# Kernel optimization log

Hardware: AMD Instinct MI355X
Metric: run time of the kernel (lower is better)

The kernel has to match this reference:

```python
import jax, jax.numpy as jnp
import numpy as np

E = 16        # num_experts
TOPK = 2      # num_experts_per_tok


def setup_inputs() -> dict:
    key = jax.random.key(0)
    ks = jax.random.split(key, 8)
    B, S, H, I, IS = 4, 2048, 1024, 512, 2048
    std = 0.02
    return {
        "hidden_states": jax.random.normal(ks[0], (B, S, H), jnp.float32),
        "gate_w": jax.random.normal(ks[1], (E, H), jnp.float32) * std,
        "gate_up_proj": jax.random.normal(ks[2], (E, 2 * I, H), jnp.float32) * std,
        "down_proj": jax.random.normal(ks[3], (E, H, I), jnp.float32) * std,
        "shared_gate_proj": jax.random.normal(ks[4], (IS, H), jnp.float32) * std,
        "shared_up_proj": jax.random.normal(ks[5], (IS, H), jnp.float32) * std,
        "shared_down_proj": jax.random.normal(ks[6], (H, IS), jnp.float32) * std,
        "shared_expert_gate_w": jax.random.normal(ks[7], (1, H), jnp.float32) * std,
    }


def _moe(x, gate_w, gate_up_proj, down_proj, sgp, sup, sdp, segw):
    # x: [N, H] flattened tokens
    N = x.shape[0]
    router_logits = x @ gate_w.T                      # [N, E]
    probs = jax.nn.softmax(router_logits, axis=-1)
    routing_weights, selected = jax.lax.top_k(probs, TOPK)   # [N, TOPK]
    routing_weights = routing_weights / routing_weights.sum(-1, keepdims=True)
    # combine weights scattered into dense [N, E] (per-token per-expert gate)
    combine = jnp.zeros((N, E), x.dtype).at[jnp.arange(N)[:, None], selected].add(routing_weights)

    def body(acc, ws):
        gu_w, d_w, cw = ws                            # [2I,H], [H,I], [N]
        gu = x @ gu_w.T                               # [N, 2I]
        g, u = jnp.split(gu, 2, axis=-1)
        h = jax.nn.silu(g) * u                        # [N, I]
        return acc + cw[:, None] * (h @ d_w.T), None

    expert_out, _ = jax.lax.scan(body, jnp.zeros_like(x), (gate_up_proj, down_proj, combine.T))

    # shared expert with sigmoid token gate
    shared_h = jax.nn.silu(x @ sgp.T) * (x @ sup.T)   # [N, IS]
    shared_out = (shared_h @ sdp.T) * jax.nn.sigmoid(x @ segw.T)  # [N, H]
    out = expert_out + shared_out

    # aux (load-balancing) loss
    counts = jnp.sum(jax.nn.one_hot(selected, E, dtype=x.dtype), axis=(0, 1))  # [E]
    frac_tokens = counts / (N * TOPK)
    frac_probs = probs.sum(0) / N
    aux_loss = E * jnp.sum(frac_tokens * frac_probs)
    return out, aux_loss


def reference(hidden_states, gate_w, gate_up_proj, down_proj, shared_gate_proj, shared_up_proj, shared_down_proj, shared_expert_gate_w):
    B, S, H = hidden_states.shape
    out, aux = _moe(hidden_states.reshape(-1, H), gate_w, gate_up_proj, down_proj,
                    shared_gate_proj, shared_up_proj, shared_down_proj, shared_expert_gate_w)
    return out.reshape(B, S, H), aux
```

## Files before the change

kernel.cpp:

```cpp
#include <hip/hip_runtime.h>
#include <hip/hip_bf16.h>
#include <stdint.h>


#define N_TOK 8192
#define HDIM 1024
#define NEXP 16
#define IEXP 512
#define ISH 2048

typedef __bf16 bf16x8 __attribute__((ext_vector_type(8)));
typedef float f32x4 __attribute__((ext_vector_type(4)));

#define OFF_XBF   ((size_t)0)
#define OFF_WSG   ((size_t)16777216)
#define OFF_WSU   ((size_t)20971520)
#define OFF_WSD   ((size_t)25165824)
#define OFF_SH    ((size_t)29360128)
#define OFF_HEXP  ((size_t)62914560)
#define OFF_IDS   ((size_t)79691776)
#define OFF_TW    ((size_t)80216064)
#define OFF_META  ((size_t)80740352)
#define OFF_SIG   ((size_t)80740608)
#define OFF_LG    ((size_t)80773376)

static __device__ __forceinline__ unsigned short f2bf(float f) {
  unsigned int u = __float_as_uint(f);
  u += 0x7fffu + ((u >> 16) & 1u);
  return (unsigned short)(u >> 16);
}
static __device__ __forceinline__ int pack_bf2(float a, float b) {
  return (int)f2bf(a) | ((int)f2bf(b) << 16);
}
static __device__ __forceinline__ void gl_lds16(const void* g, void* l) {
  __builtin_amdgcn_global_load_lds(
      (const __attribute__((address_space(1))) unsigned int*)g,
      (__attribute__((address_space(3))) unsigned int*)l, 16, 0, 0);
}

__global__ void cvt_kernel(const float* __restrict__ src,
                           unsigned short* __restrict__ dst, int n4) {
  int i = blockIdx.x * 256 + threadIdx.x;
  if (i >= n4) return;
  float4 v = ((const float4*)src)[i];
  uint2 o;
  o.x = (unsigned)pack_bf2(v.x, v.y);
  o.y = (unsigned)pack_bf2(v.z, v.w);
  ((uint2*)dst)[i] = o;
}

__global__ __launch_bounds__(256) void logits_kernel(
    const float* __restrict__ X, const float* __restrict__ GW,
    const float* __restrict__ SEGW, float* __restrict__ LG) {
  int wid = threadIdx.x >> 6, lane = threadIdx.x & 63;
  int tok = blockIdx.x * 4 + wid;
  const float* xr = X + (size_t)tok * HDIM;
  float xv[16];
#pragma unroll
  for (int i = 0; i < 16; i++) xv[i] = xr[lane + 64 * i];
  float myv = 0.f;
#pragma unroll
  for (int e = 0; e < 17; e++) {
    const float* wr = (e < 16) ? (GW + (size_t)e * HDIM) : SEGW;
    float p = 0.f;
#pragma unroll
    for (int i = 0; i < 16; i++) p += xv[i] * wr[lane + 64 * i];
#pragma unroll
    for (int off = 32; off >= 1; off >>= 1) p += __shfl_xor(p, off, 64);
    if (lane == e) myv = p;
  }
  if (lane < 17) LG[(size_t)tok * 32 + lane] = myv;
}

__global__ __launch_bounds__(256) void route_kernel(
    const float* __restrict__ LG, int* __restrict__ cnt,
    float* __restrict__ pps, int* __restrict__ ids,
    float* __restrict__ tw, float* __restrict__ sig) {
  __shared__ int lcnt[16];
  __shared__ int lbase[16];
  __shared__ float lps[16];
  int tid = threadIdx.x;
  int tok = blockIdx.x * 256 + tid;
  if (tid < 16) { lcnt[tid] = 0; lps[tid] = 0.f; }
  __syncthreads();
  const float4* row = (const float4*)(LG + (size_t)tok * 32);
  float4 v0 = row[0], v1 = row[1], v2 = row[2], v3 = row[3];
  float g16 = row[4].x;
  float lg[16] = {v0.x, v0.y, v0.z, v0.w, v1.x, v1.y, v1.z, v1.w,
                  v2.x, v2.y, v2.z, v2.w, v3.x, v3.y, v3.z, v3.w};
  float mx = lg[0];
#pragma unroll
  for (int e = 1; e < 16; e++) mx = fmaxf(mx, lg[e]);
  float pr[16], s = 0.f;
#pragma unroll
  for (int e = 0; e < 16; e++) { pr[e] = __expf(lg[e] - mx); s += pr[e]; }
  float inv_s = 1.f / s;
  float p1 = -1.f, p2 = -1.f; int i1 = 0, i2 = 0;
#pragma unroll
  for (int e = 0; e < 16; e++) {
    if (pr[e] > p1) { p2 = p1; i2 = i1; p1 = pr[e]; i1 = e; }
    else if (pr[e] > p2) { p2 = pr[e]; i2 = e; }
  }
  float wsum = p1 + p2;
  int s1 = atomicAdd(&lcnt[i1], 1);
  int s2 = atomicAdd(&lcnt[i2], 1);
#pragma unroll
  for (int e = 0; e < 16; e++) atomicAdd(&lps[e], pr[e] * inv_s);
  sig[tok] = 1.f / (1.f + __expf(-g16));
  __syncthreads();
  if (tid < 16) {
    lbase[tid] = atomicAdd(&cnt[tid], lcnt[tid]);
    atomicAdd(&pps[tid], lps[tid]);
  }
  __syncthreads();
  int d1 = i1 * N_TOK + lbase[i1] + s1;
  int d2 = i2 * N_TOK + lbase[i2] + s2;
  ids[d1] = tok; tw[d1] = p1 / wsum;
  ids[d2] = tok; tw[d2] = p2 / wsum;
}

__global__ void offs_aux_kernel(const int* __restrict__ cnt, int* __restrict__ off,
                                const float* __restrict__ probs_sum,
                                float* __restrict__ out_aux) {
  if (threadIdx.x == 0 && blockIdx.x == 0) {
    int run = 0; float aux = 0.f;
    for (int e = 0; e < NEXP; e++) {
      off[e] = run; run += cnt[e];
      aux += ((float)cnt[e] / (float)(N_TOK * 2)) * (probs_sum[e] / (float)N_TOK);
    }
    off[16] = run;
    *out_aux = (float)NEXP * aux;
  }
}

__global__ __launch_bounds__(256) void shared_gemm1_kernel(
    const unsigned short* __restrict__ X, const unsigned short* __restrict__ Wg,
    const unsigned short* __restrict__ Wu, unsigned short* __restrict__ H) {
  __shared__ __align__(16) unsigned short As[128 * 32];
  __shared__ __align__(16) unsigned short Bs1[64 * 32];
  __shared__ __align__(16) unsigned short Bs2[64 * 32];
  int m0 = blockIdx.y * 128, n0 = blockIdx.x * 64;
  int t = threadIdx.x, lane = t & 63, w = t >> 6;
  int wm = (w & 1) * 64, wn = (w >> 1) * 32;
  int arow = t >> 2, akb = (t & 3) * 8;
  const unsigned short* ap0 = X + (size_t)(m0 + arow) * HDIM + akb;
  const unsigned short* ap1 = X + (size_t)(m0 + 64 + arow) * HDIM + akb;
  const unsigned short* bp1 = Wg + (size_t)(n0 + arow) * HDIM + akb;
  const unsigned short* bp2 = Wu + (size_t)(n0 + arow) * HDIM + akb;
  f32x4 z = {0.f, 0.f, 0.f, 0.f};
  f32x4 accg[4][2], accu[4][2];
#pragma unroll
  for (int i = 0; i < 4; i++)
#pragma unroll
    for (int j = 0; j < 2; j++) { accg[i][j] = z; accu[i][j] = z; }
  for (int k0 = 0; k0 < HDIM; k0 += 32) {
    __syncthreads();
    gl_lds16(ap0 + k0, &As[t * 8]);
    gl_lds16(ap1 + k0, &As[2048 + t * 8]);
    gl_lds16(bp1 + k0, &Bs1[t * 8]);
    gl_lds16(bp2 + k0, &Bs2[t * 8]);
    __syncthreads();
    int fr = lane & 15, fc = (lane >> 4) * 8;
    bf16x8 af[4], bg[2], bu[2];
#pragma unroll
    for (int i = 0; i < 4; i++) af[i] = *(const bf16x8*)&As[(wm + i * 16 + fr) * 32 + fc];
#pragma unroll
    for (int j = 0; j < 2; j++) {
      bg[j] = *(const bf16x8*)&Bs1[(wn + j * 16 + fr) * 32 + fc];
      bu[j] = *(const bf16x8*)&Bs2[(wn + j * 16 + fr) * 32 + fc];
    }
#pragma unroll
    for (int i = 0; i < 4; i++)
#pragma unroll
      for (int j = 0; j < 2; j++) {
        accg[i][j] = __builtin_amdgcn_mfma_f32_16x16x32_bf16(af[i], bg[j], accg[i][j], 0, 0, 0);
        accu[i][j] = __builtin_amdgcn_mfma_f32_16x16x32_bf16(af[i], bu[j], accu[i][j], 0, 0, 0);
      }
  }
  int col = lane & 15, rq = (lane >> 4) * 4;
#pragma unroll
  for (int i = 0; i < 4; i++)
#pragma unroll
    for (int j = 0; j < 2; j++)
#pragma unroll
      for (int r = 0; r < 4; r++) {
        int mm = m0 + wm + i * 16 + rq + r;
        int nn = n0 + wn + j * 16 + col;
        float g = accg[i][j][r], u = accu[i][j][r];
        float h = g / (1.f + __expf(-g)) * u;
        H[(size_t)mm * ISH + nn] = f2bf(h);
      }
}

__global__ __launch_bounds__(256) void shared_gemm2_kernel(
    const unsigned short* __restrict__ H, const unsigned short* __restrict__ Wd,
    const float* __restrict__ sig, float* __restrict__ Out) {
  __shared__ __align__(16) unsigned short As[128 * 32];
  __shared__ __align__(16) unsigned short Bs[128 * 32];
  int m0 = blockIdx.y * 128, n0 = blockIdx.x * 128;
  int t = threadIdx.x, lane = t & 63, w = t >> 6;
  int wm = (w & 1) * 64, wn = (w >> 1) * 64;
  int arow = t >> 2, akb = (t & 3) * 8;
  const unsigned short* apA0 = H + (size_t)(m0 + arow) * ISH + akb;
  const unsigned short* apA1 = H + (size_t)(m0 + 64 + arow) * ISH + akb;
  const unsigned short* apB0 = Wd + (size_t)(n0 + arow) * ISH + akb;
  const unsigned short* apB1 = Wd + (size_t)(n0 + 64 + arow) * ISH + akb;
  f32x4 z = {0.f, 0.f, 0.f, 0.f};
  f32x4 acc[4][4];
#pragma unroll
  for (int i = 0; i < 4; i++)
#pragma unroll
    for (int j = 0; j < 4; j++) acc[i][j] = z;
  for (int k0 = 0; k0 < ISH; k0 += 32) {
    __syncthreads();
    gl_lds16(apA0 + k0, &As[t * 8]);
    gl_lds16(apA1 + k0, &As[2048 + t * 8]);
    gl_lds16(apB0 + k0, &Bs[t * 8]);
    gl_lds16(apB1 + k0, &Bs[2048 + t * 8]);
    __syncthreads();
    int fr = lane & 15, fc = (lane >> 4) * 8;
    bf16x8 af[4], bfr[4];
#pragma unroll
    for (int i = 0; i < 4; i++) {
      af[i] = *(const bf16x8*)&As[(wm + i * 16 + fr) * 32 + fc];
      bfr[i] = *(const bf16x8*)&Bs[(wn + i * 16 + fr) * 32 + fc];
    }
#pragma unroll
    for (int i = 0; i < 4; i++)
#pragma unroll
      for (int j = 0; j < 4; j++)
        acc[i][j] = __builtin_amdgcn_mfma_f32_16x16x32_bf16(af[i], bfr[j], acc[i][j], 0, 0, 0);
  }
  int col = lane & 15, rq = (lane >> 4) * 4;
#pragma unroll
  for (int i = 0; i < 4; i++)
#pragma unroll
    for (int r = 0; r < 4; r++) {
      int mm = m0 + wm + i * 16 + rq + r;
      float sg = sig[mm];
#pragma unroll
      for (int j = 0; j < 4; j++) {
        int nn = n0 + wn + j * 16 + col;
        Out[(size_t)mm * HDIM + nn] = acc[i][j][r] * sg;
      }
    }
}

__global__ __launch_bounds__(256) void exp_gemm1_kernel(
    const unsigned short* __restrict__ X, const float* __restrict__ WGU,
    const int* __restrict__ ids, const int* __restrict__ cnt,
    const int* __restrict__ off, unsigned short* __restrict__ Hexp) {
  int e = blockIdx.z;
  int ne = cnt[e];
  int m0 = blockIdx.y * 128;
  if (m0 >= ne) return;
  __shared__ __align__(16) unsigned short As[128 * 32];
  __shared__ __align__(16) unsigned short Bs1[64 * 32];
  __shared__ __align__(16) unsigned short Bs2[64 * 32];
  int n0 = blockIdx.x * 64;
  const int* eids = ids + e * N_TOK;
  int base = off[e];
  int t = threadIdx.x, lane = t & 63, w = t >> 6;
  int wm = (w & 1) * 64, wn = (w >> 1) * 32;
  int arow = t >> 2, akb = (t & 3) * 8;
  int s0 = m0 + arow, s1 = m0 + 64 + arow;
  int t0 = (s0 < ne) ? eids[s0] : 0;
  int t1 = (s1 < ne) ? eids[s1] : 0;
  const unsigned short* ap0 = X + (size_t)t0 * HDIM + akb;
  const unsigned short* ap1 = X + (size_t)t1 * HDIM + akb;
  const float* bpg = WGU + ((size_t)e * 1024 + n0 + arow) * HDIM + akb;
  const float* bpu = WGU + ((size_t)e * 1024 + 512 + n0 + arow) * HDIM + akb;
  f32x4 z = {0.f, 0.f, 0.f, 0.f};
  f32x4 accg[4][2], accu[4][2];
#pragma unroll
  for (int i = 0; i < 4; i++)
#pragma unroll
    for (int j = 0; j < 2; j++) { accg[i][j] = z; accu[i][j] = z; }
  for (int k0 = 0; k0 < HDIM; k0 += 32) {
    float4 g0 = *(const float4*)(bpg + k0);
    float4 g1 = *(const float4*)(bpg + k0 + 4);
    float4 u0 = *(const float4*)(bpu + k0);
    float4 u1 = *(const float4*)(bpu + k0 + 4);
    int4 b1, b2;
    b1.x = pack_bf2(g0.x, g0.y); b1.y = pack_bf2(g0.z, g0.w);
    b1.z = pack_bf2(g1.x, g1.y); b1.w = pack_bf2(g1.z, g1.w);
    b2.x = pack_bf2(u0.x, u0.y); b2.y = pack_bf2(u0.z, u0.w);
    b2.z = pack_bf2(u1.x, u1.y); b2.w = pack_bf2(u1.z, u1.w);
    __syncthreads();
    gl_lds16(ap0 + k0, &As[t * 8]);
    gl_lds16(ap1 + k0, &As[2048 + t * 8]);
    *(int4*)&Bs1[arow * 32 + akb] = b1;
    *(int4*)&Bs2[arow * 32 + akb] = b2;
    __syncthreads();
    int fr = lane & 15, fc = (lane >> 4) * 8;
    bf16x8 af[4], bg[2], bu[2];
#pragma unroll
    for (int i = 0; i < 4; i++) af[i] = *(const bf16x8*)&As[(wm + i * 16 + fr) * 32 + fc];
#pragma unroll
    for (int j = 0; j < 2; j++) {
      bg[j] = *(const bf16x8*)&Bs1[(wn + j * 16 + fr) * 32 + fc];
      bu[j] = *(const bf16x8*)&Bs2[(wn + j * 16 + fr) * 32 + fc];
    }
#pragma unroll
    for (int i = 0; i < 4; i++)
#pragma unroll
      for (int j = 0; j < 2; j++) {
        accg[i][j] = __builtin_amdgcn_mfma_f32_16x16x32_bf16(af[i], bg[j], accg[i][j], 0, 0, 0);
        accu[i][j] = __builtin_amdgcn_mfma_f32_16x16x32_bf16(af[i], bu[j], accu[i][j], 0, 0, 0);
      }
  }
  int col = lane & 15, rq = (lane >> 4) * 4;
#pragma unroll
  for (int i = 0; i < 4; i++)
#pragma unroll
    for (int j = 0; j < 2; j++)
#pragma unroll
      for (int r = 0; r < 4; r++) {
        int slot = m0 + wm + i * 16 + rq + r;
        if (slot < ne) {
          int nn = n0 + wn + j * 16 + col;
          float g = accg[i][j][r], u = accu[i][j][r];
          float h = g / (1.f + __expf(-g)) * u;
          Hexp[(size_t)(base + slot) * IEXP + nn] = f2bf(h);
        }
      }
}

__global__ __launch_bounds__(256) void exp_gemm2_kernel(
    const unsigned short* __restrict__ Hexp, const float* __restrict__ WD,
    const int* __restrict__ ids, const float* __restrict__ tw,
    const int* __restrict__ cnt, const int* __restrict__ off,
    float* __restrict__ Out) {
  int e = blockIdx.z;
  int ne = cnt[e];
  int m0 = blockIdx.y * 128;
  if (m0 >= ne) return;
  __shared__ __align__(16) unsigned short As[128 * 32];
  __shared__ __align__(16) unsigned short Bs[64 * 32];
  int n0 = blockIdx.x * 64;
  const int* eids = ids + e * N_TOK;
  const float* etw = tw + e * N_TOK;
  int base = off[e];
  int t = threadIdx.x, lane = t & 63, w = t >> 6;
  int wm = (w & 1) * 64, wn = (w >> 1) * 32;
  int arow = t >> 2, akb = (t & 3) * 8;
  int ra0 = base + m0 + arow;        if (ra0 > 16383) ra0 = 16383;
  int ra1 = base + m0 + 64 + arow;   if (ra1 > 16383) ra1 = 16383;
  const unsigned short* ap0 = Hexp + (size_t)ra0 * IEXP + akb;
  const unsigned short* ap1 = Hexp + (size_t)ra1 * IEXP + akb;
  const float* bp = WD + ((size_t)e * HDIM + n0 + arow) * IEXP + akb;
  f32x4 z = {0.f, 0.f, 0.f, 0.f};
  f32x4 acc[4][2];
#pragma unroll
  for (int i = 0; i < 4; i++)
#pragma unroll
    for (int j = 0; j < 2; j++) acc[i][j] = z;
  for (int k0 = 0; k0 < IEXP; k0 += 32) {
    float4 d0 = *(const float4*)(bp + k0);
    float4 d1 = *(const float4*)(bp + k0 + 4);
    int4 b0;
    b0.x = pack_bf2(d0.x, d0.y); b0.y = pack_bf2(d0.z, d0.w);
    b0.z = pack_bf2(d1.x, d1.y); b0.w = pack_bf2(d1.z, d1.w);
    __syncthreads();
    gl_lds16(ap0 + k0, &As[t * 8]);
    gl_lds16(ap1 + k0, &As[2048 + t * 8]);
    *(int4*)&Bs[arow * 32 + akb] = b0;
    __syncthreads();
    int fr = lane & 15, fc = (lane >> 4) * 8;
    bf16x8 af[4], bfr[2];
#pragma unroll
    for (int i = 0; i < 4; i++) af[i] = *(const bf16x8*)&As[(wm + i * 16 + fr) * 32 + fc];
#pragma unroll
    for (int j = 0; j < 2; j++) bfr[j] = *(const bf16x8*)&Bs[(wn + j * 16 + fr) * 32 + fc];
#pragma unroll
    for (int i = 0; i < 4; i++)
#pragma unroll
      for (int j = 0; j < 2; j++)
        acc[i][j] = __builtin_amdgcn_mfma_f32_16x16x32_bf16(af[i], bfr[j], acc[i][j], 0, 0, 0);
  }
  int col = lane & 15, rq = (lane >> 4) * 4;
#pragma unroll
  for (int i = 0; i < 4; i++)
#pragma unroll
    for (int r = 0; r < 4; r++) {
      int slot = m0 + wm + i * 16 + rq + r;
      if (slot < ne) {
        int tok = eids[slot];
        float wgt = etw[slot];
#pragma unroll
        for (int j = 0; j < 2; j++) {
          int nn = n0 + wn + j * 16 + col;
          atomicAdd(&Out[(size_t)tok * HDIM + nn], acc[i][j][r] * wgt);
        }
      }
    }
}

extern "C" void kernel_launch(void* const* d_in, const int* in_sizes, int n_in,
                              void* d_out, int out_size, void* d_ws, size_t ws_size,
                              hipStream_t stream) {
  const float* X   = (const float*)d_in[0];
  const float* GW  = (const float*)d_in[1];
  const float* WGU = (const float*)d_in[2];
  const float* WDN = (const float*)d_in[3];
  const float* WSG = (const float*)d_in[4];
  const float* WSU = (const float*)d_in[5];
  const float* WSD = (const float*)d_in[6];
  const float* SEGW = (const float*)d_in[7];
  float* Out = (float*)d_out;
  char* ws = (char*)d_ws;

  unsigned short* xbf  = (unsigned short*)(ws + OFF_XBF);
  unsigned short* wsg  = (unsigned short*)(ws + OFF_WSG);
  unsigned short* wsu  = (unsigned short*)(ws + OFF_WSU);
  unsigned short* wsd  = (unsigned short*)(ws + OFF_WSD);
  unsigned short* sh   = (unsigned short*)(ws + OFF_SH);
  unsigned short* hexp = (unsigned short*)(ws + OFF_HEXP);
  int*   ids  = (int*)(ws + OFF_IDS);
  float* tw   = (float*)(ws + OFF_TW);
  int*   cnt  = (int*)(ws + OFF_META);
  int*   off  = (int*)(ws + OFF_META + 64);
  float* pps  = (float*)(ws + OFF_META + 144);
  float* sig  = (float*)(ws + OFF_SIG);
  float* lg   = (float*)(ws + OFF_LG);

  hipMemsetAsync(ws + OFF_META, 0, 256, stream);

  {
    int n4;
    n4 = (N_TOK * HDIM) / 4;
    cvt_kernel<<<(n4 + 255) / 256, 256, 0, stream>>>(X, xbf, n4);
    n4 = (ISH * HDIM) / 4;
    cvt_kernel<<<(n4 + 255) / 256, 256, 0, stream>>>(WSG, wsg, n4);
    cvt_kernel<<<(n4 + 255) / 256, 256, 0, stream>>>(WSU, wsu, n4);
    n4 = (HDIM * ISH) / 4;
    cvt_kernel<<<(n4 + 255) / 256, 256, 0, stream>>>(WSD, wsd, n4);
  }

  logits_kernel<<<N_TOK / 4, 256, 0, stream>>>(X, GW, SEGW, lg);
  route_kernel<<<N_TOK / 256, 256, 0, stream>>>(lg, cnt, pps, ids, tw, sig);
  offs_aux_kernel<<<1, 64, 0, stream>>>(cnt, off, pps, Out + (size_t)N_TOK * HDIM);

  shared_gemm1_kernel<<<dim3(ISH / 64, N_TOK / 128), 256, 0, stream>>>(xbf, wsg, wsu, sh);
  shared_gemm2_kernel<<<dim3(HDIM / 128, N_TOK / 128), 256, 0, stream>>>(sh, wsd, sig, Out);

  exp_gemm1_kernel<<<dim3(IEXP / 64, N_TOK / 128, NEXP), 256, 0, stream>>>(
      xbf, WGU, ids, cnt, off, hexp);
  exp_gemm2_kernel<<<dim3(HDIM / 64, N_TOK / 128, NEXP), 256, 0, stream>>>(
      hexp, WDN, ids, tw, cnt, off, Out);
}
```

Measured before the change: 541.3 us.

## Pre-convert expert weights to bf16 and widen expert down-proj tile

Adds conversion passes that turn the expert gate/up and down weights into bf16 in workspace, reusing the shared-intermediate and x-bf16 buffers once those are no longer needed. Both expert GEMMs can then load B tiles straight into LDS with async copies instead of loading fp32 and packing to bf16 in registers on every k-step. This removes the per-block repeated fp32 weight traffic and conversion. The down-proj GEMM also widens its N tile from 64 to 128, which halves the grid and re-reads of the A tile. The cost is extra conversion kernels over 64 MB of fp32 weights and higher register use from the larger accumulator.

```diff
diff --git a/kernel.cpp b/kernel.cpp
--- a/kernel.cpp
+++ b/kernel.cpp
@@ -247,7 +247,7 @@
 }
 
 __global__ __launch_bounds__(256) void exp_gemm1_kernel(
-    const unsigned short* __restrict__ X, const float* __restrict__ WGU,
+    const unsigned short* __restrict__ X, const unsigned short* __restrict__ WGUb,
     const int* __restrict__ ids, const int* __restrict__ cnt,
     const int* __restrict__ off, unsigned short* __restrict__ Hexp) {
   int e = blockIdx.z;
@@ -268,8 +268,8 @@
   int t1 = (s1 < ne) ? eids[s1] : 0;
   const unsigned short* ap0 = X + (size_t)t0 * HDIM + akb;
   const unsigned short* ap1 = X + (size_t)t1 * HDIM + akb;
-  const float* bpg = WGU + ((size_t)e * 1024 + n0 + arow) * HDIM + akb;
-  const float* bpu = WGU + ((size_t)e * 1024 + 512 + n0 + arow) * HDIM + akb;
+  const unsigned short* bpg = WGUb + ((size_t)e * 1024 + n0 + arow) * HDIM + akb;
+  const unsigned short* bpu = WGUb + ((size_t)e * 1024 + 512 + n0 + arow) * HDIM + akb;
   f32x4 z = {0.f, 0.f, 0.f, 0.f};
   f32x4 accg[4][2], accu[4][2];
 #pragma unroll
@@ -277,20 +277,11 @@
 #pragma unroll
     for (int j = 0; j < 2; j++) { accg[i][j] = z; accu[i][j] = z; }
   for (int k0 = 0; k0 < HDIM; k0 += 32) {
-    float4 g0 = *(const float4*)(bpg + k0);
-    float4 g1 = *(const float4*)(bpg + k0 + 4);
-    float4 u0 = *(const float4*)(bpu + k0);
-    float4 u1 = *(const float4*)(bpu + k0 + 4);
-    int4 b1, b2;
-    b1.x = pack_bf2(g0.x, g0.y); b1.y = pack_bf2(g0.z, g0.w);
-    b1.z = pack_bf2(g1.x, g1.y); b1.w = pack_bf2(g1.z, g1.w);
-    b2.x = pack_bf2(u0.x, u0.y); b2.y = pack_bf2(u0.z, u0.w);
-    b2.z = pack_bf2(u1.x, u1.y); b2.w = pack_bf2(u1.z, u1.w);
     __syncthreads();
     gl_lds16(ap0 + k0, &As[t * 8]);
     gl_lds16(ap1 + k0, &As[2048 + t * 8]);
-    *(int4*)&Bs1[arow * 32 + akb] = b1;
-    *(int4*)&Bs2[arow * 32 + akb] = b2;
+    gl_lds16(bpg + k0, &Bs1[t * 8]);
+    gl_lds16(bpu + k0, &Bs2[t * 8]);
     __syncthreads();
     int fr = lane & 15, fc = (lane >> 4) * 8;
     bf16x8 af[4], bg[2], bu[2];
@@ -327,7 +318,7 @@
 }
 
 __global__ __launch_bounds__(256) void exp_gemm2_kernel(
-    const unsigned short* __restrict__ Hexp, const float* __restrict__ WD,
+    const unsigned short* __restrict__ Hexp, const unsigned short* __restrict__ WDb,
     const int* __restrict__ ids, const float* __restrict__ tw,
     const int* __restrict__ cnt, const int* __restrict__ off,
     float* __restrict__ Out) {
@@ -336,46 +327,44 @@
   int m0 = blockIdx.y * 128;
   if (m0 >= ne) return;
   __shared__ __align__(16) unsigned short As[128 * 32];
-  __shared__ __align__(16) unsigned short Bs[64 * 32];
-  int n0 = blockIdx.x * 64;
+  __shared__ __align__(16) unsigned short Bs[128 * 32];
+  int n0 = blockIdx.x * 128;
   const int* eids = ids + e * N_TOK;
   const float* etw = tw + e * N_TOK;
   int base = off[e];
   int t = threadIdx.x, lane = t & 63, w = t >> 6;
-  int wm = (w & 1) * 64, wn = (w >> 1) * 32;
+  int wm = (w & 1) * 64, wn = (w >> 1) * 64;
   int arow = t >> 2, akb = (t & 3) * 8;
   int ra0 = base + m0 + arow;        if (ra0 > 16383) ra0 = 16383;
   int ra1 = base + m0 + 64 + arow;   if (ra1 > 16383) ra1 = 16383;
   const unsigned short* ap0 = Hexp + (size_t)ra0 * IEXP + akb;
   const unsigned short* ap1 = Hexp + (size_t)ra1 * IEXP + akb;
-  const float* bp = WD + ((size_t)e * HDIM + n0 + arow) * IEXP + akb;
+  const unsigned short* bp0 = WDb + ((size_t)e * HDIM + n0 + arow) * IEXP + akb;
+  const unsigned short* bp1 = WDb + ((size_t)e * HDIM + n0 + 64 + arow) * IEXP + akb;
   f32x4 z = {0.f, 0.f, 0.f, 0.f};
-  f32x4 acc[4][2];
-#pragma unroll
-  for (int i = 0; i < 4; i++)
-#pragma unroll
-    for (int j = 0; j < 2; j++) acc[i][j] = z;
+  f32x4 acc[4][4];
+#pragma unroll
+  for (int i = 0; i < 4; i++)
+#pragma unroll
+    for (int j = 0; j < 4; j++) acc[i][j] = z;
   for (int k0 = 0; k0 < IEXP; k0 += 32) {
-    float4 d0 = *(const float4*)(bp + k0);
-    float4 d1 = *(const float4*)(bp + k0 + 4);
-    int4 b0;
-    b0.x = pack_bf2(d0.x, d0.y); b0.y = pack_bf2(d0.z, d0.w);
-    b0.z = pack_bf2(d1.x, d1.y); b0.w = pack_bf2(d1.z, d1.w);
     __syncthreads();
     gl_lds16(ap0 + k0, &As[t * 8]);
     gl_lds16(ap1 + k0, &As[2048 + t * 8]);
-    *(int4*)&Bs[arow * 32 + akb] = b0;
+    gl_lds16(bp0 + k0, &Bs[t * 8]);
+    gl_lds16(bp1 + k0, &Bs[2048 + t * 8]);
     __syncthreads();
     int fr = lane & 15, fc = (lane >> 4) * 8;
-    bf16x8 af[4], bfr[2];
-#pragma unroll
-    for (int i = 0; i < 4; i++) af[i] = *(const bf16x8*)&As[(wm + i * 16 + fr) * 32 + fc];
-#pragma unroll
-    for (int j = 0; j < 2; j++) bfr[j] = *(const bf16x8*)&Bs[(wn + j * 16 + fr) * 32 + fc];
+    bf16x8 af[4], bfr[4];
+#pragma unroll
+    for (int i = 0; i < 4; i++) {
+      af[i] = *(const bf16x8*)&As[(wm + i * 16 + fr) * 32 + fc];
+      bfr[i] = *(const bf16x8*)&Bs[(wn + i * 16 + fr) * 32 + fc];
+    }
 #pragma unroll
     for (int i = 0; i < 4; i++)
 #pragma unroll
-      for (int j = 0; j < 2; j++)
+      for (int j = 0; j < 4; j++)
         acc[i][j] = __builtin_amdgcn_mfma_f32_16x16x32_bf16(af[i], bfr[j], acc[i][j], 0, 0, 0);
   }
   int col = lane & 15, rq = (lane >> 4) * 4;
@@ -388,7 +377,7 @@
         int tok = eids[slot];
         float wgt = etw[slot];
 #pragma unroll
-        for (int j = 0; j < 2; j++) {
+        for (int j = 0; j < 4; j++) {
           int nn = n0 + wn + j * 16 + col;
           atomicAdd(&Out[(size_t)tok * HDIM + nn], acc[i][j][r] * wgt);
         }
@@ -423,6 +412,8 @@
   float* pps  = (float*)(ws + OFF_META + 144);
   float* sig  = (float*)(ws + OFF_SIG);
   float* lg   = (float*)(ws + OFF_LG);
+  unsigned short* wgu_bf = (unsigned short*)(ws + OFF_SH);
+  unsigned short* wdn_bf = (unsigned short*)(ws + OFF_XBF);
 
   hipMemsetAsync(ws + OFF_META, 0, 256, stream);
 
@@ -444,8 +435,16 @@
   shared_gemm1_kernel<<<dim3(ISH / 64, N_TOK / 128), 256, 0, stream>>>(xbf, wsg, wsu, sh);
   shared_gemm2_kernel<<<dim3(HDIM / 128, N_TOK / 128), 256, 0, stream>>>(sh, wsd, sig, Out);
 
+  {
+    int n4 = (NEXP * 2 * IEXP * HDIM) / 4;
+    cvt_kernel<<<(n4 + 255) / 256, 256, 0, stream>>>(WGU, wgu_bf, n4);
+  }
   exp_gemm1_kernel<<<dim3(IEXP / 64, N_TOK / 128, NEXP), 256, 0, stream>>>(
-      xbf, WGU, ids, cnt, off, hexp);
-  exp_gemm2_kernel<<<dim3(HDIM / 64, N_TOK / 128, NEXP), 256, 0, stream>>>(
-      hexp, WDN, ids, tw, cnt, off, Out);
-}
+      xbf, wgu_bf, ids, cnt, off, hexp);
+  {
+    int n4 = (NEXP * HDIM * IEXP) / 4;
+    cvt_kernel<<<(n4 + 255) / 256, 256, 0, stream>>>(WDN, wdn_bf, n4);
+  }
+  exp_gemm2_kernel<<<dim3(HDIM / 128, N_TOK / 128, NEXP), 256, 0, stream>>>(
+      hexp, wdn_bf, ids, tw, cnt, off, Out);
+}
```

After: 528.0 us. -2.4%, faster.
